# Kernel tuning notes

Hardware: AMD Instinct MI355X
Metric: run time of the kernel (lower is better)

Reference implementation:

```python
import jax, jax.numpy as jnp
import numpy as np

B, N, PHY, C, HID, FC, L, E = 2, 8192, 2, 64, 64, 128, 3, 524288

def _ln(x, g, b, eps=1e-5):
    mu = jnp.mean(x, axis=-1, keepdims=True)
    var = jnp.mean((x - mu) ** 2, axis=-1, keepdims=True)
    return (x - mu) * jax.lax.rsqrt(var + eps) * g + b

def setup_inputs() -> dict:
    key = jax.random.key(0)
    ks = jax.random.split(key, 24)
    s = 1.0 / np.sqrt(C)
    inp = {
        'x': jax.random.normal(ks[0], (B, N, 5), jnp.float32),
        'edge_index': jax.random.randint(ks[1], (2, E), 0, B * N, jnp.int32),
        'fc0_w': jax.random.normal(ks[2], (C, 4), jnp.float32) * 0.5,
        'fc0_b': jnp.zeros((C,), jnp.float32),
        'ln0_g': jnp.ones((C,), jnp.float32),
        'ln0_b': jnp.zeros((C,), jnp.float32),
        'gg_fc1_w': jax.random.normal(ks[3], (L, HID, C), jnp.float32) * s,
        'gg_fc1_b': jnp.zeros((L, HID), jnp.float32),
        'gg_fc2_w': jax.random.normal(ks[4], (L, C, HID), jnp.float32) * s,
        'gg_fc2_b': jnp.zeros((L, C), jnp.float32),
        'gg_weight': jax.random.uniform(ks[5], (L, HID), jnp.float32) + 0.5,
        'gg_freq': jax.random.normal(ks[6], (L, PHY, HID), jnp.float32) * (2 * np.pi),
        'wc_w': jax.random.normal(ks[7], (L, C, C), jnp.float32) * s,
        'wc_b': jnp.zeros((L, C), jnp.float32),
        'ln_g': jnp.ones((L, C), jnp.float32),
        'ln_b': jnp.zeros((L, C), jnp.float32),
        'fc1_w': jax.random.normal(ks[8], (FC, C), jnp.float32) * s,
        'fc1_b': jnp.zeros((FC,), jnp.float32),
        'fc2_w': jax.random.normal(ks[9], (1, FC), jnp.float32) / np.sqrt(FC),
        'fc2_b': jnp.zeros((1,), jnp.float32),
    }
    return inp

def reference(x, edge_index, fc0_w, fc0_b, ln0_g, ln0_b, gg_fc1_w, gg_fc1_b,
              gg_fc2_w, gg_fc2_b, gg_weight, gg_freq, wc_w, wc_b, ln_g, ln_b,
              fc1_w, fc1_b, fc2_w, fc2_b):
    grid = x[:, :, 2:4]           # (B,N,PHY): columns in_dim-phy_dim .. -1
    gw = x[:, :, 4]               # (B,N) grid_weight
    feat = x[:, :, :4]            # (B,N,in_dim)
    src, dst = edge_index[0], edge_index[1]
    grid_f = grid.reshape(-1, PHY)
    gw_f = gw.reshape(-1)
    vec = grid_f[src] - grid_f[dst]                      # (E,PHY)
    dist2 = jnp.sum(vec * vec, axis=-1, keepdims=True)   # (E,1)
    wgt_src = gw_f[src][:, None]                          # (E,1)

    h = feat @ fc0_w.T + fc0_b                            # (B,N,C)
    h = _ln(h, ln0_g, ln0_b)
    for l in range(L):
        w = gg_weight[l]                                  # (HID,)
        gauss = jnp.sqrt((w / jnp.pi) ** PHY) * jnp.exp(-w * dist2)  # (E,HID)
        fourier = jnp.sin(vec @ gg_freq[l])               # (E,HID)
        morlet = gauss * fourier
        hl = h @ gg_fc1_w[l].T + gg_fc1_b[l]              # (B,N,HID)
        val = morlet * hl.reshape(-1, HID)[src] * wgt_src # (E,HID)
        agg = jax.ops.segment_sum(val, dst, num_segments=B * N)
        x1 = agg.reshape(B, N, HID) @ gg_fc2_w[l].T + gg_fc2_b[l]
        x2 = h @ wc_w[l].T + wc_b[l]                      # pointwise Conv1d
        h = _ln(x1 + x2, ln_g[l], ln_b[l])
        if l != L - 1:
            h = jax.nn.gelu(h, approximate=False)
    h = jax.nn.gelu(h @ fc1_w.T + fc1_b, approximate=False)
    return h @ fc2_w.T + fc2_b                            # (B,N,1)
```

## Files before the change

### kernel.cpp

```cpp
#include <hip/hip_runtime.h>
#include <hip/hip_bf16.h>

#define M_NODES 16384
#define E_EDGES 524288
#define ASTR 68

typedef short short8 __attribute__((ext_vector_type(8)));
typedef float f32x4 __attribute__((ext_vector_type(4)));
typedef unsigned int uint4v __attribute__((ext_vector_type(4)));

static __device__ __forceinline__ float wredsum(float v) {
#pragma unroll
  for (int o = 32; o > 0; o >>= 1) v += __shfl_xor(v, o, 64);
  return v;
}

static __device__ __forceinline__ float gelu_exact(float x) {
  return 0.5f * x * (1.0f + erff(x * 0.70710678118654752440f));
}

static __device__ __forceinline__ unsigned int bsplit(float x) {
  unsigned int u = __float_as_uint(x);
  unsigned int hb = (u + 0x7FFFu + ((u >> 16) & 1u)) >> 16;
  float hf = __uint_as_float(hb << 16);
  float r = x - hf;
  unsigned int v = __float_as_uint(r);
  unsigned int lb = (v + 0x7FFFu + ((v >> 16) & 1u)) >> 16;
  return (hb & 0xFFFFu) | (lb << 16);
}

struct Frag { short8 hi, lo; };

static __device__ __forceinline__ Frag load_afrag(const unsigned int* a) {
  uint4v u0 = *(const uint4v*)a;
  uint4v u1 = *(const uint4v*)(a + 4);
  Frag f;
#pragma unroll
  for (int j = 0; j < 4; ++j) {
    f.hi[j]     = (short)(u0[j] & 0xFFFFu);
    f.lo[j]     = (short)(u0[j] >> 16);
    f.hi[j + 4] = (short)(u1[j] & 0xFFFFu);
    f.lo[j + 4] = (short)(u1[j] >> 16);
  }
  return f;
}

static __device__ __forceinline__ Frag load_bfrag(const float* __restrict__ w) {
  float4 w0 = *(const float4*)w;
  float4 w1 = *(const float4*)(w + 4);
  float v[8] = {w0.x, w0.y, w0.z, w0.w, w1.x, w1.y, w1.z, w1.w};
  Frag f;
#pragma unroll
  for (int j = 0; j < 8; ++j) {
    unsigned int p = bsplit(v[j]);
    f.hi[j] = (short)(p & 0xFFFFu);
    f.lo[j] = (short)(p >> 16);
  }
  return f;
}

static __device__ __forceinline__ f32x4 mfma3(const Frag& a, const Frag& b, f32x4 c) {
  c = __builtin_amdgcn_mfma_f32_16x16x32_bf16(a.hi, b.hi, c, 0, 0, 0);
  c = __builtin_amdgcn_mfma_f32_16x16x32_bf16(a.lo, b.hi, c, 0, 0, 0);
  c = __builtin_amdgcn_mfma_f32_16x16x32_bf16(a.hi, b.lo, c, 0, 0, 0);
  return c;
}

static __device__ __forceinline__ f32x4 gemm16(const unsigned int* __restrict__ A,
                                               const float* __restrict__ W,
                                               int n, int c, int q) {
  Frag a0 = load_afrag(A + c * ASTR + 8 * q);
  Frag a1 = load_afrag(A + c * ASTR + 32 + 8 * q);
  Frag b0 = load_bfrag(W + n * 64 + 8 * q);
  Frag b1 = load_bfrag(W + n * 64 + 32 + 8 * q);
  f32x4 acc = {0.f, 0.f, 0.f, 0.f};
  acc = mfma3(a0, b0, acc);
  acc = mfma3(a1, b1, acc);
  return acc;
}

__global__ __launch_bounds__(256) void k_init(
    const float* __restrict__ x,
    const float* __restrict__ fc0_w, const float* __restrict__ fc0_b,
    const float* __restrict__ ln0_g, const float* __restrict__ ln0_b,
    const float* __restrict__ w1, const float* __restrict__ b1,
    const float* __restrict__ wc, const float* __restrict__ wcb,
    float2* __restrict__ grid2, float* __restrict__ gwf,
    float* __restrict__ hl, float* __restrict__ x2)
{
  __shared__ unsigned int A[16 * ASTR];
  const int tid = threadIdx.x, lane = tid & 63, w = tid >> 6;
  const int tilebase = blockIdx.x * 16;

  float fw0 = fc0_w[lane * 4 + 0], fw1 = fc0_w[lane * 4 + 1];
  float fw2v = fc0_w[lane * 4 + 2], fw3 = fc0_w[lane * 4 + 3];
  float fb = fc0_b[lane], g0 = ln0_g[lane], bb0 = ln0_b[lane];

#pragma unroll
  for (int i = 0; i < 4; ++i) {
    int node = tilebase + 4 * w + i;
    float xv0 = x[node * 5 + 0], xv1 = x[node * 5 + 1], xv2 = x[node * 5 + 2];
    float xv3 = x[node * 5 + 3], xv4 = x[node * 5 + 4];
    float acc = fb + xv0 * fw0 + xv1 * fw1 + xv2 * fw2v + xv3 * fw3;
    float mean = wredsum(acc) * (1.0f / 64.0f);
    float d = acc - mean;
    float var = wredsum(d * d) * (1.0f / 64.0f);
    float hv = d * rsqrtf(var + 1e-5f) * g0 + bb0;
    A[(4 * w + i) * ASTR + lane] = bsplit(hv);
    if (lane == 0) { grid2[node] = make_float2(xv2, xv3); gwf[node] = xv4; }
  }
  __syncthreads();

  const int c = lane & 15, q = lane >> 4;
  const int n = 16 * w + c;

  f32x4 a1v = gemm16(A, w1, n, c, q);
  float b1v = b1[n];
#pragma unroll
  for (int r = 0; r < 4; ++r)
    hl[(tilebase + 4 * q + r) * 64 + n] = a1v[r] + b1v;

  f32x4 a2v = gemm16(A, wc, n, c, q);
  float wcbv = wcb[n];
#pragma unroll
  for (int r = 0; r < 4; ++r)
    x2[(tilebase + 4 * q + r) * 64 + n] = a2v[r] + wcbv;
}

__global__ __launch_bounds__(256) void k_count(const int* __restrict__ ei, int* __restrict__ cnt)
{
  int e = blockIdx.x * 256 + threadIdx.x;
  if (e < E_EDGES) atomicAdd(&cnt[ei[E_EDGES + e]], 1);
}

__global__ __launch_bounds__(1024) void k_scan(const int* __restrict__ cnt,
                                               int* __restrict__ row_start,
                                               int* __restrict__ cursor)
{
  const int PER = M_NODES / 1024;
  const int t = threadIdx.x;
  const int base = t * PER;
  int local[PER];
  int s = 0;
#pragma unroll
  for (int k = 0; k < PER; ++k) { local[k] = cnt[base + k]; s += local[k]; }

  __shared__ int part[1024];
  part[t] = s;
  __syncthreads();
  for (int off = 1; off < 1024; off <<= 1) {
    int v = (t >= off) ? part[t - off] : 0;
    __syncthreads();
    part[t] += v;
    __syncthreads();
  }
  int run = part[t] - s;
#pragma unroll
  for (int k = 0; k < PER; ++k) {
    row_start[base + k] = run;
    cursor[base + k] = run;
    run += local[k];
  }
  if (t == 1023) row_start[M_NODES] = run;
}

__global__ __launch_bounds__(256) void k_scatter(
    const int* __restrict__ ei, const float2* __restrict__ grid2,
    const float* __restrict__ gwf, int* __restrict__ cursor,
    float4* __restrict__ rec)
{
  int e = blockIdx.x * 256 + threadIdx.x;
  if (e < E_EDGES) {
    int s = ei[e];
    int dd = ei[E_EDGES + e];
    int pos = atomicAdd(&cursor[dd], 1);
    float2 gs = grid2[s], gd = grid2[dd];
    rec[pos] = make_float4(gs.x - gd.x, gs.y - gd.y, gwf[s], __int_as_float(s));
  }
}

__global__ __launch_bounds__(256) void k_agg(
    const float4* __restrict__ rec, const int* __restrict__ row_start,
    const float* __restrict__ hl,
    const float* __restrict__ gw, const float* __restrict__ freq,
    float* __restrict__ agg)
{
  const int lane = threadIdx.x & 63;
  const int node = blockIdx.x * 4 + (threadIdx.x >> 6);

  const float w = gw[lane];
  const float nwl2 = -w * 1.44269504088896340736f;
  const float lc = log2f(w * 0.31830988618379067154f);
  const float f0s = freq[lane] * 0.15915494309189533577f;
  const float f1s = freq[64 + lane] * 0.15915494309189533577f;

  const int beg = row_start[node];
  const int end = row_start[node + 1];
  float acc = 0.0f;

  int i = beg;
  if (i < end) {
    float4 r = rec[i];
    float hlv = hl[__float_as_int(r.w) * 64 + lane];
    for (++i; i < end; ++i) {
      float4 rn = rec[i];
      float hn = hl[__float_as_int(rn.w) * 64 + lane];
      float dist2 = r.x * r.x + r.y * r.y;
      float gs = __builtin_amdgcn_exp2f(__builtin_fmaf(nwl2, dist2, lc));
      float rev = __builtin_fmaf(r.x, f0s, r.y * f1s);
      float fo = __builtin_amdgcn_sinf(__builtin_amdgcn_fractf(rev));
      acc = __builtin_fmaf(gs * fo * hlv, r.z, acc);
      r = rn; hlv = hn;
    }
    float dist2 = r.x * r.x + r.y * r.y;
    float gs = __builtin_amdgcn_exp2f(__builtin_fmaf(nwl2, dist2, lc));
    float rev = __builtin_fmaf(r.x, f0s, r.y * f1s);
    float fo = __builtin_amdgcn_sinf(__builtin_amdgcn_fractf(rev));
    acc = __builtin_fmaf(gs * fo * hlv, r.z, acc);
  }
  agg[node * 64 + lane] = acc;
}

__global__ __launch_bounds__(256) void k_post_mid(
    const float* __restrict__ agg,
    const float* __restrict__ w2, const float* __restrict__ b2,
    const float* __restrict__ lng, const float* __restrict__ lnb,
    const float* __restrict__ nw1, const float* __restrict__ nb1,
    const float* __restrict__ nwc, const float* __restrict__ nwcb,
    float* __restrict__ hl, float* __restrict__ x2)
{
  __shared__ unsigned int A[16 * ASTR];
  __shared__ float PS[4][16], PQ[4][16];
  const int tid = threadIdx.x, lane = tid & 63, w = tid >> 6;
  const int tilebase = blockIdx.x * 16;
  const int c = lane & 15, q = lane >> 4;
  const int n = 16 * w + c;

  float x2v[4];
#pragma unroll
  for (int r = 0; r < 4; ++r)
    x2v[r] = x2[(tilebase + 4 * q + r) * 64 + n];
  float lg = lng[n], lb = lnb[n], vb = b2[n];

  {
    int i = tid * 4;
    int row = i >> 6, col = i & 63;
    float4 v = *(const float4*)(agg + tilebase * 64 + i);
    uint4v pv;
    pv[0] = bsplit(v.x); pv[1] = bsplit(v.y); pv[2] = bsplit(v.z); pv[3] = bsplit(v.w);
    *(uint4v*)(A + row * ASTR + col) = pv;
  }
  __syncthreads();

  f32x4 acc = gemm16(A, w2, n, c, q);

  float S[4];
#pragma unroll
  for (int r = 0; r < 4; ++r) S[r] = acc[r] + vb + x2v[r];

#pragma unroll
  for (int r = 0; r < 4; ++r) {
    float s1 = S[r], s2 = S[r] * S[r];
#pragma unroll
    for (int m = 1; m < 16; m <<= 1) {
      s1 += __shfl_xor(s1, m, 64);
      s2 += __shfl_xor(s2, m, 64);
    }
    if (c == 0) { PS[w][4 * q + r] = s1; PQ[w][4 * q + r] = s2; }
  }
  __syncthreads();

#pragma unroll
  for (int r = 0; r < 4; ++r) {
    int row = 4 * q + r;
    float sum = PS[0][row] + PS[1][row] + PS[2][row] + PS[3][row];
    float sq  = PQ[0][row] + PQ[1][row] + PQ[2][row] + PQ[3][row];
    float mean = sum * (1.0f / 64.0f);
    float var = sq * (1.0f / 64.0f) - mean * mean;
    float hv = (S[r] - mean) * rsqrtf(var + 1e-5f) * lg + lb;
    hv = gelu_exact(hv);
    A[row * ASTR + n] = bsplit(hv);
  }
  __syncthreads();

  f32x4 a1v = gemm16(A, nw1, n, c, q);
  float b1v = nb1[n];
#pragma unroll
  for (int r = 0; r < 4; ++r)
    hl[(tilebase + 4 * q + r) * 64 + n] = a1v[r] + b1v;

  f32x4 a2v = gemm16(A, nwc, n, c, q);
  float wcbv = nwcb[n];
#pragma unroll
  for (int r = 0; r < 4; ++r)
    x2[(tilebase + 4 * q + r) * 64 + n] = a2v[r] + wcbv;
}

__global__ __launch_bounds__(256) void k_post_last(
    const float* __restrict__ agg,
    const float* __restrict__ w2, const float* __restrict__ b2,
    const float* __restrict__ lng, const float* __restrict__ lnb,
    const float* __restrict__ x2,
    const float* __restrict__ fc1w, const float* __restrict__ fc1b,
    const float* __restrict__ fw2, const float* __restrict__ fb2,
    float* __restrict__ out)
{
  __shared__ unsigned int A[16 * ASTR];
  __shared__ float PS[4][16], PQ[4][16];
  const int tid = threadIdx.x, lane = tid & 63, w = tid >> 6;
  const int tilebase = blockIdx.x * 16;
  const int c = lane & 15, q = lane >> 4;
  const int n = 16 * w + c;

  float x2v[4];
#pragma unroll
  for (int r = 0; r < 4; ++r)
    x2v[r] = x2[(tilebase + 4 * q + r) * 64 + n];
  float lg = lng[n], lb = lnb[n], vb = b2[n];

  {
    int i = tid * 4;
    int row = i >> 6, col = i & 63;
    float4 v = *(const float4*)(agg + tilebase * 64 + i);
    uint4v pv;
    pv[0] = bsplit(v.x); pv[1] = bsplit(v.y); pv[2] = bsplit(v.z); pv[3] = bsplit(v.w);
    *(uint4v*)(A + row * ASTR + col) = pv;
  }
  __syncthreads();

  f32x4 acc = gemm16(A, w2, n, c, q);

  float S[4];
#pragma unroll
  for (int r = 0; r < 4; ++r) S[r] = acc[r] + vb + x2v[r];

#pragma unroll
  for (int r = 0; r < 4; ++r) {
    float s1 = S[r], s2 = S[r] * S[r];
#pragma unroll
    for (int m = 1; m < 16; m <<= 1) {
      s1 += __shfl_xor(s1, m, 64);
      s2 += __shfl_xor(s2, m, 64);
    }
    if (c == 0) { PS[w][4 * q + r] = s1; PQ[w][4 * q + r] = s2; }
  }
  __syncthreads();

#pragma unroll
  for (int r = 0; r < 4; ++r) {
    int row = 4 * q + r;
    float sum = PS[0][row] + PS[1][row] + PS[2][row] + PS[3][row];
    float sq  = PQ[0][row] + PQ[1][row] + PQ[2][row] + PQ[3][row];
    float mean = sum * (1.0f / 64.0f);
    float var = sq * (1.0f / 64.0f) - mean * mean;
    float hv = (S[r] - mean) * rsqrtf(var + 1e-5f) * lg + lb;
    A[row * ASTR + n] = bsplit(hv);
  }
  __syncthreads();

  Frag ha0 = load_afrag(A + c * ASTR + 8 * q);
  Frag ha1 = load_afrag(A + c * ASTR + 32 + 8 * q);
  float p[4] = {0.f, 0.f, 0.f, 0.f};
#pragma unroll
  for (int half = 0; half < 2; ++half) {
    int row = 32 * w + 16 * half + c;
    Frag b0 = load_bfrag(fc1w + row * 64 + 8 * q);
    Frag b1 = load_bfrag(fc1w + row * 64 + 32 + 8 * q);
    f32x4 a = {0.f, 0.f, 0.f, 0.f};
    a = mfma3(ha0, b0, a);
    a = mfma3(ha1, b1, a);
    float fbv = fc1b[row], fwv = fw2[row];
#pragma unroll
    for (int r = 0; r < 4; ++r) p[r] += gelu_exact(a[r] + fbv) * fwv;
  }
#pragma unroll
  for (int r = 0; r < 4; ++r) {
    float s = p[r];
#pragma unroll
    for (int m = 1; m < 16; m <<= 1) s += __shfl_xor(s, m, 64);
    if (c == 0) PS[w][4 * q + r] = s;
  }
  __syncthreads();
  if (tid < 16)
    out[tilebase + tid] = PS[0][tid] + PS[1][tid] + PS[2][tid] + PS[3][tid] + fb2[0];
}

extern "C" void kernel_launch(void* const* d_in, const int* in_sizes, int n_in,
                              void* d_out, int out_size, void* d_ws, size_t ws_size,
                              hipStream_t stream) {
  const float* x     = (const float*)d_in[0];
  const int* ei      = (const int*)d_in[1];
  const float* fc0_w = (const float*)d_in[2];
  const float* fc0_b = (const float*)d_in[3];
  const float* ln0_g = (const float*)d_in[4];
  const float* ln0_b = (const float*)d_in[5];
  const float* gg_fc1_w = (const float*)d_in[6];
  const float* gg_fc1_b = (const float*)d_in[7];
  const float* gg_fc2_w = (const float*)d_in[8];
  const float* gg_fc2_b = (const float*)d_in[9];
  const float* gg_weight = (const float*)d_in[10];
  const float* gg_freq   = (const float*)d_in[11];
  const float* wc_w = (const float*)d_in[12];
  const float* wc_b = (const float*)d_in[13];
  const float* ln_g = (const float*)d_in[14];
  const float* ln_b = (const float*)d_in[15];
  const float* fc1_w = (const float*)d_in[16];
  const float* fc1_b = (const float*)d_in[17];
  const float* fc2_w = (const float*)d_in[18];
  const float* fc2_b = (const float*)d_in[19];

  char* ws = (char*)d_ws;
  size_t off = 0;
  auto alloc = [&](size_t bytes) -> void* {
    void* p = ws + off;
    off = (off + bytes + 255) & ~(size_t)255;
    return p;
  };
  float2* grid2   = (float2*)alloc((size_t)M_NODES * 8);
  float*  gwf     = (float*)alloc((size_t)M_NODES * 4);
  float*  hl      = (float*)alloc((size_t)M_NODES * 64 * 4);
  float*  agg     = (float*)alloc((size_t)M_NODES * 64 * 4);
  float*  x2      = (float*)alloc((size_t)M_NODES * 64 * 4);
  int*    cnt     = (int*)alloc((size_t)M_NODES * 4);
  int*    cursor  = (int*)alloc((size_t)M_NODES * 4);
  int*    row_st  = (int*)alloc((size_t)(M_NODES + 1) * 4);
  float4* rec     = (float4*)alloc((size_t)E_EDGES * 16);
  (void)ws_size; (void)in_sizes; (void)n_in; (void)out_size;

  hipMemsetAsync(cnt, 0, (size_t)M_NODES * 4, stream);

  k_init<<<M_NODES / 16, 256, 0, stream>>>(x, fc0_w, fc0_b, ln0_g, ln0_b,
                                           gg_fc1_w, gg_fc1_b, wc_w, wc_b,
                                           grid2, gwf, hl, x2);
  k_count<<<E_EDGES / 256, 256, 0, stream>>>(ei, cnt);
  k_scan<<<1, 1024, 0, stream>>>(cnt, row_st, cursor);
  k_scatter<<<E_EDGES / 256, 256, 0, stream>>>(ei, grid2, gwf, cursor, rec);

  for (int l = 0; l < 3; ++l) {
    k_agg<<<M_NODES / 4, 256, 0, stream>>>(rec, row_st, hl,
                                           gg_weight + l * 64, gg_freq + l * 128, agg);
    if (l < 2) {
      k_post_mid<<<M_NODES / 16, 256, 0, stream>>>(
          agg,
          gg_fc2_w + l * 4096, gg_fc2_b + l * 64,
          ln_g + l * 64, ln_b + l * 64,
          gg_fc1_w + (l + 1) * 4096, gg_fc1_b + (l + 1) * 64,
          wc_w + (l + 1) * 4096, wc_b + (l + 1) * 64,
          hl, x2);
    } else {
      k_post_last<<<M_NODES / 16, 256, 0, stream>>>(
          agg,
          gg_fc2_w + l * 4096, gg_fc2_b + l * 64,
          ln_g + l * 64, ln_b + l * 64,
          x2,
          fc1_w, fc1_b, fc2_w, fc2_b,
          (float*)d_out);
    }
  }
}
```

Baseline: 288.0 us.

## Fuse init/count/weight-packing kernel, batch edge loads in agg, prepack bf16 weights

Merges the init, edge-count and a new weight pre-split (bf16 hi/lo packing) into one launch using block-index ranges. The aggregation kernel now stages 64 edge records per chunk in LDS and double-buffers groups of 8 gathers ahead of the transcendental math, and it writes agg already split into bf16 hi/lo pairs. x2 is stored transposed for float4 access. The post kernels load pre-packed weights instead of splitting them per block. This removes a launch and redundant bsplit work and raises memory-level parallelism in the gather. The cost is extra register pressure and a more complex kernel.

```diff
diff --git a/kernel.cpp b/kernel.cpp
--- a/kernel.cpp
+++ b/kernel.cpp
@@ -8,6 +8,12 @@
 typedef short short8 __attribute__((ext_vector_type(8)));
 typedef float f32x4 __attribute__((ext_vector_type(4)));
 typedef unsigned int uint4v __attribute__((ext_vector_type(4)));
+
+#define PK_W1 0
+#define PK_WC 12288
+#define PK_W2 24576
+#define PK_FC1 36864
+#define PK_TOTAL 45056
 
 static __device__ __forceinline__ float wredsum(float v) {
 #pragma unroll
@@ -66,31 +72,63 @@
   return c;
 }
 
-static __device__ __forceinline__ f32x4 gemm16(const unsigned int* __restrict__ A,
-                                               const float* __restrict__ W,
-                                               int n, int c, int q) {
+static __device__ __forceinline__ Frag load_bpk(const short* __restrict__ P, int S, int n, int off) {
+  Frag f;
+  f.hi = *(const short8*)(P + n * 64 + off);
+  f.lo = *(const short8*)(P + S + n * 64 + off);
+  return f;
+}
+
+static __device__ __forceinline__ f32x4 gemm16p(const unsigned int* __restrict__ A,
+                                                const short* __restrict__ P, int S,
+                                                int n, int c, int q) {
   Frag a0 = load_afrag(A + c * ASTR + 8 * q);
   Frag a1 = load_afrag(A + c * ASTR + 32 + 8 * q);
-  Frag b0 = load_bfrag(W + n * 64 + 8 * q);
-  Frag b1 = load_bfrag(W + n * 64 + 32 + 8 * q);
+  Frag b0 = load_bpk(P, S, n, 8 * q);
+  Frag b1 = load_bpk(P, S, n, 32 + 8 * q);
   f32x4 acc = {0.f, 0.f, 0.f, 0.f};
   acc = mfma3(a0, b0, acc);
   acc = mfma3(a1, b1, acc);
   return acc;
 }
 
-__global__ __launch_bounds__(256) void k_init(
+__global__ __launch_bounds__(256) void k_front(
     const float* __restrict__ x,
     const float* __restrict__ fc0_w, const float* __restrict__ fc0_b,
     const float* __restrict__ ln0_g, const float* __restrict__ ln0_b,
-    const float* __restrict__ w1, const float* __restrict__ b1,
-    const float* __restrict__ wc, const float* __restrict__ wcb,
+    const float* __restrict__ gg_fc1_w, const float* __restrict__ gg_fc1_b,
+    const float* __restrict__ wc_w, const float* __restrict__ wc_b,
+    const float* __restrict__ gg_fc2_w, const float* __restrict__ fc1_w,
+    const int* __restrict__ ei, int* __restrict__ cnt, short* __restrict__ pk,
     float2* __restrict__ grid2, float* __restrict__ gwf,
-    float* __restrict__ hl, float* __restrict__ x2)
+    float* __restrict__ hl, float* __restrict__ x2T)
 {
   __shared__ unsigned int A[16 * ASTR];
-  const int tid = threadIdx.x, lane = tid & 63, w = tid >> 6;
-  const int tilebase = blockIdx.x * 16;
+  const int bid = blockIdx.x;
+  const int tid = threadIdx.x;
+
+  if (bid >= 3072) {
+    int i = (bid - 3072) * 256 + tid;
+    float v = (i < PK_WC)  ? gg_fc1_w[i]
+            : (i < PK_W2)  ? wc_w[i - PK_WC]
+            : (i < PK_FC1) ? gg_fc2_w[i - PK_W2]
+                           : fc1_w[i - PK_FC1];
+    int mb, sz;
+    if (i < PK_FC1) { mb = i & ~4095; sz = 4096; } else { mb = PK_FC1; sz = 8192; }
+    int k = i - mb;
+    unsigned int p = bsplit(v);
+    pk[2 * mb + k]      = (short)(p & 0xFFFFu);
+    pk[2 * mb + sz + k] = (short)(p >> 16);
+    return;
+  }
+  if (bid >= 1024) {
+    int e = (bid - 1024) * 256 + tid;
+    atomicAdd(&cnt[ei[E_EDGES + e]], 1);
+    return;
+  }
+
+  const int lane = tid & 63, w = tid >> 6;
+  const int tilebase = bid * 16;
 
   float fw0 = fc0_w[lane * 4 + 0], fw1 = fc0_w[lane * 4 + 1];
   float fw2v = fc0_w[lane * 4 + 2], fw3 = fc0_w[lane * 4 + 3];
@@ -114,23 +152,28 @@
   const int c = lane & 15, q = lane >> 4;
   const int n = 16 * w + c;
 
-  f32x4 a1v = gemm16(A, w1, n, c, q);
-  float b1v = b1[n];
-#pragma unroll
-  for (int r = 0; r < 4; ++r)
-    hl[(tilebase + 4 * q + r) * 64 + n] = a1v[r] + b1v;
-
-  f32x4 a2v = gemm16(A, wc, n, c, q);
-  float wcbv = wcb[n];
-#pragma unroll
-  for (int r = 0; r < 4; ++r)
-    x2[(tilebase + 4 * q + r) * 64 + n] = a2v[r] + wcbv;
-}
-
-__global__ __launch_bounds__(256) void k_count(const int* __restrict__ ei, int* __restrict__ cnt)
-{
-  int e = blockIdx.x * 256 + threadIdx.x;
-  if (e < E_EDGES) atomicAdd(&cnt[ei[E_EDGES + e]], 1);
+  {
+    Frag a0 = load_afrag(A + c * ASTR + 8 * q);
+    Frag a1 = load_afrag(A + c * ASTR + 32 + 8 * q);
+    Frag b0 = load_bfrag(gg_fc1_w + n * 64 + 8 * q);
+    Frag b1 = load_bfrag(gg_fc1_w + n * 64 + 32 + 8 * q);
+    f32x4 acc = {0.f, 0.f, 0.f, 0.f};
+    acc = mfma3(a0, b0, acc);
+    acc = mfma3(a1, b1, acc);
+    float b1v = gg_fc1_b[n];
+#pragma unroll
+    for (int r = 0; r < 4; ++r)
+      hl[(tilebase + 4 * q + r) * 64 + n] = acc[r] + b1v;
+
+    Frag c0 = load_bfrag(wc_w + n * 64 + 8 * q);
+    Frag c1 = load_bfrag(wc_w + n * 64 + 32 + 8 * q);
+    f32x4 ac2 = {0.f, 0.f, 0.f, 0.f};
+    ac2 = mfma3(a0, c0, ac2);
+    ac2 = mfma3(a1, c1, ac2);
+    float wcbv = wc_b[n];
+    *(float4*)(x2T + n * M_NODES + tilebase + 4 * q) =
+        make_float4(ac2[0] + wcbv, ac2[1] + wcbv, ac2[2] + wcbv, ac2[3] + wcbv);
+  }
 }
 
 __global__ __launch_bounds__(1024) void k_scan(const int* __restrict__ cnt,
@@ -183,51 +226,83 @@
     const float4* __restrict__ rec, const int* __restrict__ row_start,
     const float* __restrict__ hl,
     const float* __restrict__ gw, const float* __restrict__ freq,
-    float* __restrict__ agg)
+    unsigned int* __restrict__ aggp)
 {
+  __shared__ float4 LR[4][64];
   const int lane = threadIdx.x & 63;
-  const int node = blockIdx.x * 4 + (threadIdx.x >> 6);
-
-  const float w = gw[lane];
-  const float nwl2 = -w * 1.44269504088896340736f;
-  const float lc = log2f(w * 0.31830988618379067154f);
+  const int w = threadIdx.x >> 6;
+  const int node = blockIdx.x * 4 + w;
+
+  const float wv = gw[lane];
+  const float nwl2 = -wv * 1.44269504088896340736f;
+  const float lc = log2f(wv * 0.31830988618379067154f);
   const float f0s = freq[lane] * 0.15915494309189533577f;
   const float f1s = freq[64 + lane] * 0.15915494309189533577f;
 
   const int beg = row_start[node];
   const int end = row_start[node + 1];
+  const float* hlp = hl + lane;
+  float4* LRw = LR[w];
+
   float acc = 0.0f;
 
-  int i = beg;
-  if (i < end) {
-    float4 r = rec[i];
-    float hlv = hl[__float_as_int(r.w) * 64 + lane];
-    for (++i; i < end; ++i) {
-      float4 rn = rec[i];
-      float hn = hl[__float_as_int(rn.w) * 64 + lane];
-      float dist2 = r.x * r.x + r.y * r.y;
-      float gs = __builtin_amdgcn_exp2f(__builtin_fmaf(nwl2, dist2, lc));
-      float rev = __builtin_fmaf(r.x, f0s, r.y * f1s);
-      float fo = __builtin_amdgcn_sinf(__builtin_amdgcn_fractf(rev));
-      acc = __builtin_fmaf(gs * fo * hlv, r.z, acc);
-      r = rn; hlv = hn;
+  for (int base = beg; base < end; base += 64) {
+    const int cn = min(64, end - base);
+    if (lane < cn) LRw[lane] = rec[base + lane];
+
+    float4 RA[8], RB[8];
+    float HA[8], HB[8];
+
+    auto ldg = [&](float4* R, float* H, int off) {
+#pragma unroll
+      for (int u = 0; u < 8; ++u) {
+        int j = off + u; j = (j < cn) ? j : (cn - 1);
+        R[u] = LRw[j];
+      }
+#pragma unroll
+      for (int u = 0; u < 8; ++u)
+        H[u] = hlp[__float_as_int(R[u].w) * 64];
+    };
+    auto cmp8 = [&](const float4* R, const float* H, int off) {
+#pragma unroll
+      for (int u = 0; u < 8; ++u) {
+        if (off + u < cn) {
+          float dist2 = __builtin_fmaf(R[u].x, R[u].x, R[u].y * R[u].y);
+          float gs = __builtin_amdgcn_exp2f(__builtin_fmaf(nwl2, dist2, lc));
+          float rev = __builtin_fmaf(R[u].x, f0s, R[u].y * f1s);
+          float fo = __builtin_amdgcn_sinf(__builtin_amdgcn_fractf(rev));
+          acc = __builtin_fmaf(gs * fo * H[u], R[u].z, acc);
+        }
+      }
+    };
+
+    const int Gp = (cn + 7) >> 3;
+    ldg(RA, HA, 0);
+    int g = 0;
+    for (; g + 2 < Gp; g += 2) {
+      ldg(RB, HB, 8 * (g + 1));
+      cmp8(RA, HA, 8 * g);
+      ldg(RA, HA, 8 * (g + 2));
+      cmp8(RB, HB, 8 * (g + 1));
     }
-    float dist2 = r.x * r.x + r.y * r.y;
-    float gs = __builtin_amdgcn_exp2f(__builtin_fmaf(nwl2, dist2, lc));
-    float rev = __builtin_fmaf(r.x, f0s, r.y * f1s);
-    float fo = __builtin_amdgcn_sinf(__builtin_amdgcn_fractf(rev));
-    acc = __builtin_fmaf(gs * fo * hlv, r.z, acc);
-  }
-  agg[node * 64 + lane] = acc;
+    if (g + 1 < Gp) {
+      ldg(RB, HB, 8 * (g + 1));
+      cmp8(RA, HA, 8 * g);
+      cmp8(RB, HB, 8 * (g + 1));
+    } else {
+      cmp8(RA, HA, 8 * g);
+    }
+  }
+  aggp[node * 64 + lane] = bsplit(acc);
 }
 
 __global__ __launch_bounds__(256) void k_post_mid(
-    const float* __restrict__ agg,
-    const float* __restrict__ w2, const float* __restrict__ b2,
+    const unsigned int* __restrict__ aggp,
+    const short* __restrict__ pw2, const float* __restrict__ b2,
     const float* __restrict__ lng, const float* __restrict__ lnb,
-    const float* __restrict__ nw1, const float* __restrict__ nb1,
-    const float* __restrict__ nwc, const float* __restrict__ nwcb,
-    float* __restrict__ hl, float* __restrict__ x2)
+    const short* __restrict__ pnw1, const float* __restrict__ nb1,
+    const short* __restrict__ pnwc, const float* __restrict__ nwcb,
+    float* __restrict__ hl, float* __restrict__ x2T)
 {
   __shared__ unsigned int A[16 * ASTR];
   __shared__ float PS[4][16], PQ[4][16];
@@ -236,23 +311,23 @@
   const int c = lane & 15, q = lane >> 4;
   const int n = 16 * w + c;
 
-  float x2v[4];
-#pragma unroll
-  for (int r = 0; r < 4; ++r)
-    x2v[r] = x2[(tilebase + 4 * q + r) * 64 + n];
+  float4 x2v = *(const float4*)(x2T + n * M_NODES + tilebase + 4 * q);
   float lg = lng[n], lb = lnb[n], vb = b2[n];
+  float b1v = nb1[n], wcbv = nwcb[n];
+  Frag wb0 = load_bpk(pw2, 4096, n, 8 * q);
+  Frag wb1 = load_bpk(pw2, 4096, n, 32 + 8 * q);
 
   {
     int i = tid * 4;
-    int row = i >> 6, col = i & 63;
-    float4 v = *(const float4*)(agg + tilebase * 64 + i);
-    uint4v pv;
-    pv[0] = bsplit(v.x); pv[1] = bsplit(v.y); pv[2] = bsplit(v.z); pv[3] = bsplit(v.w);
-    *(uint4v*)(A + row * ASTR + col) = pv;
-  }
-  __syncthreads();
-
-  f32x4 acc = gemm16(A, w2, n, c, q);
+    *(uint4v*)(A + (i >> 6) * ASTR + (i & 63)) = *(const uint4v*)(aggp + tilebase * 64 + i);
+  }
+  __syncthreads();
+
+  Frag a0 = load_afrag(A + c * ASTR + 8 * q);
+  Frag a1 = load_afrag(A + c * ASTR + 32 + 8 * q);
+  f32x4 acc = {0.f, 0.f, 0.f, 0.f};
+  acc = mfma3(a0, wb0, acc);
+  acc = mfma3(a1, wb1, acc);
 
   float S[4];
 #pragma unroll
@@ -283,25 +358,22 @@
   }
   __syncthreads();
 
-  f32x4 a1v = gemm16(A, nw1, n, c, q);
-  float b1v = nb1[n];
+  f32x4 h1 = gemm16p(A, pnw1, 4096, n, c, q);
 #pragma unroll
   for (int r = 0; r < 4; ++r)
-    hl[(tilebase + 4 * q + r) * 64 + n] = a1v[r] + b1v;
-
-  f32x4 a2v = gemm16(A, nwc, n, c, q);
-  float wcbv = nwcb[n];
-#pragma unroll
-  for (int r = 0; r < 4; ++r)
-    x2[(tilebase + 4 * q + r) * 64 + n] = a2v[r] + wcbv;
+    hl[(tilebase + 4 * q + r) * 64 + n] = h1[r] + b1v;
+
+  f32x4 hx = gemm16p(A, pnwc, 4096, n, c, q);
+  *(float4*)(x2T + n * M_NODES + tilebase + 4 * q) =
+      make_float4(hx[0] + wcbv, hx[1] + wcbv, hx[2] + wcbv, hx[3] + wcbv);
 }
 
 __global__ __launch_bounds__(256) void k_post_last(
-    const float* __restrict__ agg,
-    const float* __restrict__ w2, const float* __restrict__ b2,
+    const unsigned int* __restrict__ aggp,
+    const short* __restrict__ pw2, const float* __restrict__ b2,
     const float* __restrict__ lng, const float* __restrict__ lnb,
-    const float* __restrict__ x2,
-    const float* __restrict__ fc1w, const float* __restrict__ fc1b,
+    const float* __restrict__ x2T,
+    const short* __restrict__ pfc1, const float* __restrict__ fc1b,
     const float* __restrict__ fw2, const float* __restrict__ fb2,
     float* __restrict__ out)
 {
@@ -312,23 +384,22 @@
   const int c = lane & 15, q = lane >> 4;
   const int n = 16 * w + c;
 
-  float x2v[4];
-#pragma unroll
-  for (int r = 0; r < 4; ++r)
-    x2v[r] = x2[(tilebase + 4 * q + r) * 64 + n];
+  float4 x2v = *(const float4*)(x2T + n * M_NODES + tilebase + 4 * q);
   float lg = lng[n], lb = lnb[n], vb = b2[n];
+  Frag wb0 = load_bpk(pw2, 4096, n, 8 * q);
+  Frag wb1 = load_bpk(pw2, 4096, n, 32 + 8 * q);
 
   {
     int i = tid * 4;
-    int row = i >> 6, col = i & 63;
-    float4 v = *(const float4*)(agg + tilebase * 64 + i);
-    uint4v pv;
-    pv[0] = bsplit(v.x); pv[1] = bsplit(v.y); pv[2] = bsplit(v.z); pv[3] = bsplit(v.w);
-    *(uint4v*)(A + row * ASTR + col) = pv;
-  }
-  __syncthreads();
-
-  f32x4 acc = gemm16(A, w2, n, c, q);
+    *(uint4v*)(A + (i >> 6) * ASTR + (i & 63)) = *(const uint4v*)(aggp + tilebase * 64 + i);
+  }
+  __syncthreads();
+
+  Frag a0 = load_afrag(A + c * ASTR + 8 * q);
+  Frag a1 = load_afrag(A + c * ASTR + 32 + 8 * q);
+  f32x4 acc = {0.f, 0.f, 0.f, 0.f};
+  acc = mfma3(a0, wb0, acc);
+  acc = mfma3(a1, wb1, acc);
 
   float S[4];
 #pragma unroll
@@ -364,8 +435,8 @@
 #pragma unroll
   for (int half = 0; half < 2; ++half) {
     int row = 32 * w + 16 * half + c;
-    Frag b0 = load_bfrag(fc1w + row * 64 + 8 * q);
-    Frag b1 = load_bfrag(fc1w + row * 64 + 32 + 8 * q);
+    Frag b0 = load_bpk(pfc1, 8192, row, 8 * q);
+    Frag b1 = load_bpk(pfc1, 8192, row, 32 + 8 * q);
     f32x4 a = {0.f, 0.f, 0.f, 0.f};
     a = mfma3(ha0, b0, a);
     a = mfma3(ha1, b1, a);
@@ -416,44 +487,44 @@
     off = (off + bytes + 255) & ~(size_t)255;
     return p;
   };
-  float2* grid2   = (float2*)alloc((size_t)M_NODES * 8);
-  float*  gwf     = (float*)alloc((size_t)M_NODES * 4);
-  float*  hl      = (float*)alloc((size_t)M_NODES * 64 * 4);
-  float*  agg     = (float*)alloc((size_t)M_NODES * 64 * 4);
-  float*  x2      = (float*)alloc((size_t)M_NODES * 64 * 4);
-  int*    cnt     = (int*)alloc((size_t)M_NODES * 4);
-  int*    cursor  = (int*)alloc((size_t)M_NODES * 4);
-  int*    row_st  = (int*)alloc((size_t)(M_NODES + 1) * 4);
-  float4* rec     = (float4*)alloc((size_t)E_EDGES * 16);
+  float2* grid2 = (float2*)alloc((size_t)M_NODES * 8);
+  float*  gwf   = (float*)alloc((size_t)M_NODES * 4);
+  float*  hl    = (float*)alloc((size_t)M_NODES * 64 * 4);
+  unsigned int* aggp = (unsigned int*)alloc((size_t)M_NODES * 64 * 4);
+  float*  x2T   = (float*)alloc((size_t)M_NODES * 64 * 4);
+  int*    cnt   = (int*)alloc((size_t)M_NODES * 4);
+  int*    cursor= (int*)alloc((size_t)M_NODES * 4);
+  int*    row_st= (int*)alloc((size_t)(M_NODES + 1) * 4);
+  float4* rec   = (float4*)alloc((size_t)E_EDGES * 16);
+  short*  pk    = (short*)alloc((size_t)PK_TOTAL * 2 * 2);
   (void)ws_size; (void)in_sizes; (void)n_in; (void)out_size;
 
   hipMemsetAsync(cnt, 0, (size_t)M_NODES * 4, stream);
 
-  k_init<<<M_NODES / 16, 256, 0, stream>>>(x, fc0_w, fc0_b, ln0_g, ln0_b,
-                                           gg_fc1_w, gg_fc1_b, wc_w, wc_b,
-                                           grid2, gwf, hl, x2);
-  k_count<<<E_EDGES / 256, 256, 0, stream>>>(ei, cnt);
+  k_front<<<3248, 256, 0, stream>>>(x, fc0_w, fc0_b, ln0_g, ln0_b,
+                                    gg_fc1_w, gg_fc1_b, wc_w, wc_b,
+                                    gg_fc2_w, fc1_w,
+                                    ei, cnt, pk, grid2, gwf, hl, x2T);
   k_scan<<<1, 1024, 0, stream>>>(cnt, row_st, cursor);
   k_scatter<<<E_EDGES / 256, 256, 0, stream>>>(ei, grid2, gwf, cursor, rec);
 
   for (int l = 0; l < 3; ++l) {
     k_agg<<<M_NODES / 4, 256, 0, stream>>>(rec, row_st, hl,
-                                           gg_weight + l * 64, gg_freq + l * 128, agg);
+                                           gg_weight + l * 64, gg_freq + l * 128, aggp);
+    const short* pw2 = pk + 2 * (PK_W2 + l * 4096);
     if (l < 2) {
       k_post_mid<<<M_NODES / 16, 256, 0, stream>>>(
-          agg,
-          gg_fc2_w + l * 4096, gg_fc2_b + l * 64,
+          aggp, pw2, gg_fc2_b + l * 64,
           ln_g + l * 64, ln_b + l * 64,
-          gg_fc1_w + (l + 1) * 4096, gg_fc1_b + (l + 1) * 64,
-          wc_w + (l + 1) * 4096, wc_b + (l + 1) * 64,
-          hl, x2);
+          pk + 2 * (PK_W1 + (l + 1) * 4096), gg_fc1_b + (l + 1) * 64,
+          pk + 2 * (PK_WC + (l + 1) * 4096), wc_b + (l + 1) * 64,
+          hl, x2T);
     } else {
       k_post_last<<<M_NODES / 16, 256, 0, stream>>>(
-          agg,
-          gg_fc2_w + l * 4096, gg_fc2_b + l * 64,
+          aggp, pw2, gg_fc2_b + l * 64,
           ln_g + l * 64, ln_b + l * 64,
-          x2,
-          fc1_w, fc1_b, fc2_w, fc2_b,
+          x2T,
+          pk + 2 * PK_FC1, fc1_b, fc2_w, fc2_b,
           (float*)d_out);
     }
   }
```

New measurement: 260.5 us. 9.5% less time.
